# Performance work log

Measured on AMD Instinct MI355X. Metric: run time of the kernel, lower is better.

## Reference

```python
import jax, jax.numpy as jnp
import numpy as np

FRACTION_BITS = 16
INTEGER_BITS = 16


def round_to_fixed(x):
    # floor-quantize to 2^-16 steps, clamp to signed 16-bit integer range
    delta = 2.0 ** (-FRACTION_BITS)
    bound = 2.0 ** (INTEGER_BITS - 1)
    return jnp.clip(jnp.floor(x / delta) * delta, -bound, bound - 1.0)


def setup_inputs() -> dict:
    key = jax.random.key(0)
    k1, k2, k3, k4 = jax.random.split(key, 4)
    N, IN_F, OUT_F = 4096, 4096, 4096
    inp = jax.random.normal(k1, (N, IN_F), dtype=jnp.float32)
    # reset_parameters: shift ~ U(-10,-1), sign ~ U(-1,0), bias ~ U(-b,b), b=1/sqrt(fan_in)
    shift = jax.random.uniform(k2, (OUT_F, IN_F), minval=-10.0, maxval=-1.0, dtype=jnp.float32)
    sign = jax.random.uniform(k3, (OUT_F, IN_F), minval=-1.0, maxval=0.0, dtype=jnp.float32)
    b = 1.0 / np.sqrt(IN_F)
    bias = jax.random.uniform(k4, (OUT_F,), minval=-b, maxval=b, dtype=jnp.float32)
    return {"input": inp, "shift": shift, "sign": sign, "bias": bias}


def reference(input, shift, sign, bias):
    # eager (non-kernel) path of LinearShiftFunction.forward
    q_in = round_to_fixed(input)
    q_bias = round_to_fixed(bias)
    s = jnp.clip(sign, -1.0, 1.0)
    v = jnp.exp2(jnp.round(shift)) * jnp.sign(s)  # [out_f, in_f] power-of-two weights
    out = q_in @ v.T + q_bias[None, :]
    return out
```

## Files before the change

kernel.cpp:

```cpp
#include <hip/hip_runtime.h>
#include <hip/hip_bf16.h>


#define BM 256
#define BN 128
#define BK 32

typedef __bf16 bf16_t;
typedef __attribute__((ext_vector_type(8))) __bf16 bf16x8;
typedef __attribute__((ext_vector_type(4))) __bf16 bf16x4;
typedef __attribute__((ext_vector_type(4))) float f32x4;

__device__ __forceinline__ float q16(float x) {
    float f = floorf(x * 65536.0f) * (1.0f / 65536.0f);
    return fminf(fmaxf(f, -32768.0f), 32767.0f);
}

__global__ void quant_input_kernel(const float* __restrict__ in,
                                   bf16_t* __restrict__ out, int nvec) {
    int stride = gridDim.x * blockDim.x;
    for (int i = blockIdx.x * blockDim.x + threadIdx.x; i < nvec; i += stride) {
        float4 v = reinterpret_cast<const float4*>(in)[i];
        bf16x4 o;
        o[0] = (bf16_t)q16(v.x);
        o[1] = (bf16_t)q16(v.y);
        o[2] = (bf16_t)q16(v.z);
        o[3] = (bf16_t)q16(v.w);
        reinterpret_cast<bf16x4*>(out)[i] = o;
    }
}

__global__ void make_weight_kernel(const float* __restrict__ shift,
                                   const float* __restrict__ sign_,
                                   bf16_t* __restrict__ out, int nvec) {
    int stride = gridDim.x * blockDim.x;
    for (int i = blockIdx.x * blockDim.x + threadIdx.x; i < nvec; i += stride) {
        float4 sh = reinterpret_cast<const float4*>(shift)[i];
        float4 sg = reinterpret_cast<const float4*>(sign_)[i];
        float shs[4] = {sh.x, sh.y, sh.z, sh.w};
        float sgs[4] = {sg.x, sg.y, sg.z, sg.w};
        bf16x4 o;
#pragma unroll
        for (int j = 0; j < 4; ++j) {
            float s = fminf(fmaxf(sgs[j], -1.0f), 1.0f);
            float sv = (s > 0.0f) ? 1.0f : ((s < 0.0f) ? -1.0f : 0.0f);
            o[j] = (bf16_t)(exp2f(rintf(shs[j])) * sv);
        }
        reinterpret_cast<bf16x4*>(out)[i] = o;
    }
}


#define VMW(N) asm volatile("s_waitcnt vmcnt(" #N ")" ::: "memory")
#define BARF() do { __builtin_amdgcn_s_barrier(); asm volatile("" ::: "memory"); } while (0)

#define GLDS(SRC, DST)                                                                   \
    __builtin_amdgcn_global_load_lds(                                                    \
        (const __attribute__((address_space(1))) void*)(SRC),                            \
        (__attribute__((address_space(3))) void*)(DST), 16, 0, 0)

#define STAGE_TILE(SB, T) do {                                                           \
    _Pragma("unroll") for (int i = 0; i < 4; ++i)                                        \
        GLDS(srcA + (size_t)(i * 64) * K + (size_t)(T) * 32,                             \
             &lds[(SB) + i * 2048] + tid * 8);                                           \
    _Pragma("unroll") for (int i = 0; i < 2; ++i)                                        \
        GLDS(srcB + (size_t)(i * 64) * K + (size_t)(T) * 32,                             \
             &lds[(SB) + 8192 + i * 2048] + tid * 8);                                    \
} while (0)

#define READ_FRAGS(RB) do {                                                              \
    _Pragma("unroll") for (int m = 0; m < 8; ++m)                                        \
        af[m] = *(const bf16x8*)&lds[(RB) + (wm * 64 + m * 8 + prw) * 64 + sl8];         \
    _Pragma("unroll") for (int n = 0; n < 4; ++n)                                        \
        bf[n] = *(const bf16x8*)&lds[(RB) + 8192 + (wn * 32 + n * 8 + prw) * 64 + sl8];  \
} while (0)

#define MFMA32() do {                                                                    \
    __builtin_amdgcn_s_setprio(1);                                                       \
    _Pragma("unroll") for (int m = 0; m < 8; ++m)                                        \
        _Pragma("unroll") for (int n = 0; n < 4; ++n)                                    \
            acc[m][n] = __builtin_amdgcn_mfma_f32_16x16x32_bf16(                         \
                af[m], bf[n], acc[m][n], 0, 0, 0);                                       \
    __builtin_amdgcn_s_setprio(0);                                                       \
} while (0)

__global__ __launch_bounds__(256, 2)
void gemm256_kernel(const bf16_t* __restrict__ A,
                    const bf16_t* __restrict__ B,
                    const float* __restrict__ bias,
                    float* __restrict__ C,
                    int M, int N, int K) {
    __shared__ bf16_t lds[36864];

    const int ntn = N / BN;
    const int nwg = gridDim.x;
    const int q = nwg >> 3, r = nwg & 7;
    const int xcd = blockIdx.x & 7, lid = blockIdx.x >> 3;
    const int swz = (xcd < r ? xcd * (q + 1) : r * (q + 1) + (xcd - r) * q) + lid;
    const int tile_m = (swz / ntn) * BM;
    const int tile_n = (swz % ntn) * BN;

    const int tid = threadIdx.x;
    const int lane = tid & 63;
    const int wid = tid >> 6;
    const int wm = wid >> 1;
    const int wn = wid & 1;
    const int fr = lane & 15;
    const int hi = lane >> 4;
    const int prw = fr >> 1;
    const int sl8 = ((((fr & 1) << 2) | hi) ^ ((fr >> 1) & 3)) << 3;

    const int sraw = (tid & 7) ^ ((tid >> 3) & 3);
    const int rloc = 2 * (tid >> 3) + (sraw >> 2);
    const int kloc = (sraw & 3) << 3;
    const bf16_t* srcA = A + (size_t)(tile_m + rloc) * K + kloc;
    const bf16_t* srcB = B + (size_t)(tile_n + rloc) * K + kloc;

    bf16x8 af[8], bf[4];
    f32x4 acc[8][4] = {};

    STAGE_TILE(0, 0);
    STAGE_TILE(12288, 1);
    VMW(6);
    BARF();

    int rb = 0, rb1 = 12288, rb2 = 24576;
    for (int t = 0; t < 128; ++t) {
        READ_FRAGS(rb);
        if (t < 126) STAGE_TILE(rb2, t + 2);
        MFMA32();
        if (t < 126) VMW(6);
        else if (t == 126) VMW(0);
        if (t < 127) BARF();
        const int tmp = rb; rb = rb1; rb1 = rb2; rb2 = tmp;
    }

    float qb[4];
#pragma unroll
    for (int n = 0; n < 4; ++n)
        qb[n] = q16(bias[tile_n + wn * 64 + n * 16 + fr]);
#pragma unroll
    for (int m = 0; m < 8; ++m) {
        const int grow0 = tile_m + wm * 128 + m * 16 + hi * 4;
#pragma unroll
        for (int n = 0; n < 4; ++n) {
            const int gcol = tile_n + wn * 64 + n * 16 + fr;
#pragma unroll
            for (int rr = 0; rr < 4; ++rr)
                C[(size_t)(grow0 + rr) * N + gcol] = acc[m][n][rr] + qb[n];
        }
    }
}

extern "C" void kernel_launch(void* const* d_in, const int* in_sizes, int n_in,
                              void* d_out, int out_size, void* d_ws, size_t ws_size,
                              hipStream_t stream) {
    const float* inp   = (const float*)d_in[0];
    const float* shift = (const float*)d_in[1];
    const float* sign_ = (const float*)d_in[2];
    const float* bias  = (const float*)d_in[3];
    float* out = (float*)d_out;

    const int OUT_F = in_sizes[3];
    const int IN_F  = in_sizes[1] / OUT_F;
    const int Mrows = in_sizes[0] / IN_F;

    bf16_t* Aq = (bf16_t*)d_ws;
    bf16_t* Wq = Aq + (size_t)Mrows * IN_F;

    const int nA = Mrows * IN_F;
    const int nW = OUT_F * IN_F;

    quant_input_kernel<<<2048, 256, 0, stream>>>(inp, Aq, nA >> 2);
    make_weight_kernel<<<2048, 256, 0, stream>>>(shift, sign_, Wq, nW >> 2);

    dim3 grid((Mrows / BM) * (OUT_F / BN));
    gemm256_kernel<<<grid, 256, 0, stream>>>(Aq, Wq, bias, out,
                                             Mrows, OUT_F, IN_F);
}
```

Before: 182.4 us.

## Enlarge GEMM tile to 256x256 with 8 waves, 4-stage pipeline, fused conversion

The GEMM tile grows from 256x128 to 256x256, run by 512 threads (8 waves in a 2x4 layout). Each block now stages the A and B tiles with 4 global-to-LDS loads per thread. The pipeline deepens from 3 to 4 LDS buffers with an unrolled loop and explicit vmcnt waits, and the two preprocessing kernels merge into one launch. The goal is more operand reuse per byte loaded and fewer launches. In exchange the block needs 128KB of LDS, so at most one block fits per CU despite launch_bounds(512,2), which reduces occupancy. The fused conversion also assumes the input and weight tensors are the same size.

```diff
diff --git a/kernel.cpp b/kernel.cpp
--- a/kernel.cpp
+++ b/kernel.cpp
@@ -3,8 +3,7 @@
 
 
 #define BM 256
-#define BN 128
-#define BK 32
+#define BN 256
 
 typedef __bf16 bf16_t;
 typedef __attribute__((ext_vector_type(8))) __bf16 bf16x8;
@@ -16,37 +15,33 @@
     return fminf(fmaxf(f, -32768.0f), 32767.0f);
 }
 
-__global__ void quant_input_kernel(const float* __restrict__ in,
-                                   bf16_t* __restrict__ out, int nvec) {
+__global__ void convert_kernel(const float* __restrict__ in,
+                               const float* __restrict__ shift,
+                               const float* __restrict__ sign_,
+                               bf16_t* __restrict__ aq,
+                               bf16_t* __restrict__ wq, int nvec) {
     int stride = gridDim.x * blockDim.x;
     for (int i = blockIdx.x * blockDim.x + threadIdx.x; i < nvec; i += stride) {
         float4 v = reinterpret_cast<const float4*>(in)[i];
-        bf16x4 o;
-        o[0] = (bf16_t)q16(v.x);
-        o[1] = (bf16_t)q16(v.y);
-        o[2] = (bf16_t)q16(v.z);
-        o[3] = (bf16_t)q16(v.w);
-        reinterpret_cast<bf16x4*>(out)[i] = o;
-    }
-}
+        bf16x4 oa;
+        oa[0] = (bf16_t)q16(v.x);
+        oa[1] = (bf16_t)q16(v.y);
+        oa[2] = (bf16_t)q16(v.z);
+        oa[3] = (bf16_t)q16(v.w);
+        reinterpret_cast<bf16x4*>(aq)[i] = oa;
 
-__global__ void make_weight_kernel(const float* __restrict__ shift,
-                                   const float* __restrict__ sign_,
-                                   bf16_t* __restrict__ out, int nvec) {
-    int stride = gridDim.x * blockDim.x;
-    for (int i = blockIdx.x * blockDim.x + threadIdx.x; i < nvec; i += stride) {
         float4 sh = reinterpret_cast<const float4*>(shift)[i];
         float4 sg = reinterpret_cast<const float4*>(sign_)[i];
         float shs[4] = {sh.x, sh.y, sh.z, sh.w};
         float sgs[4] = {sg.x, sg.y, sg.z, sg.w};
-        bf16x4 o;
+        bf16x4 ow;
 #pragma unroll
         for (int j = 0; j < 4; ++j) {
             float s = fminf(fmaxf(sgs[j], -1.0f), 1.0f);
             float sv = (s > 0.0f) ? 1.0f : ((s < 0.0f) ? -1.0f : 0.0f);
-            o[j] = (bf16_t)(exp2f(rintf(shs[j])) * sv);
+            ow[j] = (bf16_t)(exp2f(rintf(shs[j])) * sv);
         }
-        reinterpret_cast<bf16x4*>(out)[i] = o;
+        reinterpret_cast<bf16x4*>(wq)[i] = ow;
     }
 }
 
@@ -59,13 +54,11 @@
         (const __attribute__((address_space(1))) void*)(SRC),                            \
         (__attribute__((address_space(3))) void*)(DST), 16, 0, 0)
 
-#define STAGE_TILE(SB, T) do {                                                           \
-    _Pragma("unroll") for (int i = 0; i < 4; ++i)                                        \
-        GLDS(srcA + (size_t)(i * 64) * K + (size_t)(T) * 32,                             \
-             &lds[(SB) + i * 2048] + tid * 8);                                           \
-    _Pragma("unroll") for (int i = 0; i < 2; ++i)                                        \
-        GLDS(srcB + (size_t)(i * 64) * K + (size_t)(T) * 32,                             \
-             &lds[(SB) + 8192 + i * 2048] + tid * 8);                                    \
+#define STAGE_TILE(RB, T) do {                                                           \
+    GLDS(srcA + (size_t)(T) * 32,                 &lds[(RB)] + tid * 8);                 \
+    GLDS(srcA + (size_t)128 * K + (size_t)(T) * 32, &lds[(RB) + 4096] + tid * 8);        \
+    GLDS(srcB + (size_t)(T) * 32,                 &lds[(RB) + 8192] + tid * 8);          \
+    GLDS(srcB + (size_t)128 * K + (size_t)(T) * 32, &lds[(RB) + 12288] + tid * 8);       \
 } while (0)
 
 #define READ_FRAGS(RB) do {                                                              \
@@ -84,13 +77,23 @@
     __builtin_amdgcn_s_setprio(0);                                                       \
 } while (0)
 
-__global__ __launch_bounds__(256, 2)
+#define TILE(RB, T, DOS, W, DOBAR) do {                                                  \
+    READ_FRAGS(RB);                                                                      \
+    if (DOS) STAGE_TILE((((RB) + 49152) % 65536), (T) + 3);                              \
+    MFMA32();                                                                            \
+    if ((W) == 8) VMW(8);                                                                \
+    else if ((W) == 4) VMW(4);                                                           \
+    else if ((W) == 0) VMW(0);                                                           \
+    if (DOBAR) BARF();                                                                   \
+} while (0)
+
+__global__ __launch_bounds__(512, 2)
 void gemm256_kernel(const bf16_t* __restrict__ A,
                     const bf16_t* __restrict__ B,
                     const float* __restrict__ bias,
                     float* __restrict__ C,
                     int M, int N, int K) {
-    __shared__ bf16_t lds[36864];
+    __shared__ bf16_t lds[65536];
 
     const int ntn = N / BN;
     const int nwg = gridDim.x;
@@ -103,8 +106,8 @@
     const int tid = threadIdx.x;
     const int lane = tid & 63;
     const int wid = tid >> 6;
-    const int wm = wid >> 1;
-    const int wn = wid & 1;
+    const int wm = wid >> 2;
+    const int wn = wid & 3;
     const int fr = lane & 15;
     const int hi = lane >> 4;
     const int prw = fr >> 1;
@@ -120,20 +123,21 @@
     f32x4 acc[8][4] = {};
 
     STAGE_TILE(0, 0);
-    STAGE_TILE(12288, 1);
-    VMW(6);
+    STAGE_TILE(16384, 1);
+    STAGE_TILE(32768, 2);
+    VMW(8);
     BARF();
 
-    int rb = 0, rb1 = 12288, rb2 = 24576;
-    for (int t = 0; t < 128; ++t) {
-        READ_FRAGS(rb);
-        if (t < 126) STAGE_TILE(rb2, t + 2);
-        MFMA32();
-        if (t < 126) VMW(6);
-        else if (t == 126) VMW(0);
-        if (t < 127) BARF();
-        const int tmp = rb; rb = rb1; rb1 = rb2; rb2 = tmp;
+    for (int i = 0; i < 31; ++i) {
+        TILE(0,     4 * i,     1, 8, 1);
+        TILE(16384, 4 * i + 1, 1, 8, 1);
+        TILE(32768, 4 * i + 2, 1, 8, 1);
+        TILE(49152, 4 * i + 3, 1, 8, 1);
     }
+    TILE(0,     124, 1, 8, 1);
+    TILE(16384, 125, 0, 4, 1);
+    TILE(32768, 126, 0, 0, 1);
+    TILE(49152, 127, 0, -1, 0);
 
     float qb[4];
 #pragma unroll
@@ -169,12 +173,10 @@
     bf16_t* Wq = Aq + (size_t)Mrows * IN_F;
 
     const int nA = Mrows * IN_F;
-    const int nW = OUT_F * IN_F;
 
-    quant_input_kernel<<<2048, 256, 0, stream>>>(inp, Aq, nA >> 2);
-    make_weight_kernel<<<2048, 256, 0, stream>>>(shift, sign_, Wq, nW >> 2);
+    convert_kernel<<<2048, 256, 0, stream>>>(inp, shift, sign_, Aq, Wq, nA >> 2);
 
     dim3 grid((Mrows / BM) * (OUT_F / BN));
-    gemm256_kernel<<<grid, 256, 0, stream>>>(Aq, Wq, bias, out,
+    gemm256_kernel<<<grid, 512, 0, stream>>>(Aq, Wq, bias, out,
                                              Mrows, OUT_F, IN_F);
 }
```

Measured after the change: 162.2 us. 1.12x faster.
